# Kernel optimization log

Measured on AMD Instinct MI355X. Metric: run time of the kernel, lower is better.

Reference implementation:

```python
import jax, jax.numpy as jnp
import numpy as np
from jax import lax

# Model dims (match init_kwargs)
B, CX, XS = 32, 3, 64          # batch, x_channels, x_size
CY, K, S, Z = 32, 10, 1, 256   # y_channels, kernel_size, stride, z_size
M = (XS - K) // S + 1          # y_size = 55
FEAT = CY * M * M              # flattened y feature size
DT, TAU_X, TAU_Y = 0.1, 1.0, 0.2
BETA_Y, BETA_Z = 3.0, 7.0
STEPS = 30                     # max_num_steps
DN = ('NCHW', 'OIHW', 'NCHW')


def setup_inputs() -> dict:
    key = jax.random.key(0)
    k1, k2, k3 = jax.random.split(key, 3)
    x = jax.random.normal(k1, (B, CX, XS, XS), dtype=jnp.float32)
    # conv/convT share this kernel (torch ties convT.weight = conv.weight)
    Kw = jax.random.normal(k2, (CY, CX, K, K), dtype=jnp.float32) / np.sqrt(CX * K * K)
    # xavier_normal_ for W [Z, FEAT]
    W = jax.random.normal(k3, (Z, FEAT), dtype=jnp.float32) * np.sqrt(2.0 / (Z + FEAT))
    return {"x": x, "Kw": Kw, "W": W}


def _step(x, y, Kw, W):
    # fc: z = W @ softmax_channels(beta_y * y).flatten  -> [B, Z]
    fy = jax.nn.softmax(BETA_Y * y, axis=1)                       # softmax over channel dim
    z = jnp.einsum('zf,bf->bz', W, fy.reshape(fy.shape[0], -1))
    # nonlin_z: softmax over z-slots (dim=-2 of [B,N,1] == N axis)
    fz = jax.nn.softmax(BETA_Z * z, axis=-1)
    top = jnp.einsum('zf,bz->bf', W, fz).reshape(-1, CY, M, M)    # fcT
    conv_x = lax.conv_general_dilated(x, Kw, (S, S), 'VALID', dimension_numbers=DN)
    y_inst = conv_x + top
    y = y + DT / TAU_Y * (-y + y_inst)
    # x_instant = convT(softmax_channels(y))  (no beta here, matching the torch code)
    x_inst = lax.conv_transpose(jax.nn.softmax(y, axis=1), Kw, (S, S), 'VALID',
                                dimension_numbers=DN, transpose_kernel=True)
    x = x + DT / TAU_X * (-x + x_inst)
    return x, y


def reference(x, Kw, W):
    y0 = jnp.zeros((x.shape[0], CY, M, M), dtype=x.dtype)

    def body(carry, _):
        xc, yc = carry
        return _step(xc, yc, Kw, W), None

    (xf, _), _ = lax.scan(body, (x, y0), None, length=STEPS)
    return xf
```

## Files before the change

kernel.cpp:

```cpp
#include <hip/hip_runtime.h>

#define K_B    32
#define K_CXC  3
#define K_XS   64
#define K_CY   32
#define K_M    55
#define K_Z    256
#define K_P    (K_M*K_M)
#define K_FEAT (K_CY*K_P)
#define K_XN   (K_CXC*K_XS*K_XS)
#define K_NSPLIT 55

typedef __attribute__((ext_vector_type(8))) short short8;
typedef __attribute__((ext_vector_type(4))) float f32x4;

__device__ __forceinline__ short f2bf(float f) {
    unsigned u = __builtin_bit_cast(unsigned, f);
    unsigned r = (u + 0x7FFFu + ((u >> 16) & 1u)) >> 16;
    return (short)r;
}

__global__ __launch_bounds__(256) void w_to_bf16(const float* __restrict__ W,
                                                 short* __restrict__ Wb) {
    size_t i = ((size_t)blockIdx.x*256 + threadIdx.x) * 8;
    float4 a = *(const float4*)(W + i);
    float4 b = *(const float4*)(W + i + 4);
    short8 o;
    o[0]=f2bf(a.x); o[1]=f2bf(a.y); o[2]=f2bf(a.z); o[3]=f2bf(a.w);
    o[4]=f2bf(b.x); o[5]=f2bf(b.y); o[6]=f2bf(b.z); o[7]=f2bf(b.w);
    *(short8*)(Wb + i) = o;
}

__global__ __launch_bounds__(256) void w_to_g2(const float* __restrict__ W,
                                               short* __restrict__ Wg2) {
    int f = blockIdx.x*256 + threadIdx.x;
    if (f >= K_FEAT) return;
    int zb = blockIdx.y;
    short8 o;
    #pragma unroll
    for (int j = 0; j < 8; ++j) o[j] = f2bf(W[(size_t)(zb*8 + j)*K_FEAT + f]);
    *(short8*)(Wg2 + ((size_t)zb*K_FEAT + f)*8) = o;
}

__global__ __launch_bounds__(256) void prep_frags(const float* __restrict__ Kw,
                                                  short* __restrict__ KfragT,
                                                  short* __restrict__ Kfrag2) {
    int e = blockIdx.x*256 + threadIdx.x;
    if (e < 6400) {
        int uv = e >> 6, l = e & 63;
        int u = uv / 10, v = uv - u*10;
        int lr = l & 15, lg = l >> 4;
        short8 o;
        #pragma unroll
        for (int j = 0; j < 8; ++j) {
            int cy = lg*8 + j;
            o[j] = (lr < 3) ? f2bf(Kw[cy*300 + lr*100 + (9-u)*10 + (9-v)]) : (short)0;
        }
        *(short8*)(KfragT + (size_t)e*8) = o;
    } else if (e < 6400 + 1920) {
        int e2 = e - 6400;
        int kn = e2 >> 6, l = e2 & 63;
        int ks = kn >> 1, nt = kn & 1;
        int lr = l & 15, lg = l >> 4;
        short8 o;
        #pragma unroll
        for (int j = 0; j < 8; ++j) {
            int k = ks*32 + lg*8 + j;
            int cx = k / 160, rem = k - cx*160;
            int u = rem >> 4, v = rem & 15;
            o[j] = (v < 10) ? f2bf(Kw[(lr + nt*16)*300 + cx*100 + u*10 + v]) : (short)0;
        }
        *(short8*)(Kfrag2 + (size_t)e2*8) = o;
    }
}

__global__ __launch_bounds__(256) void fyb_fill(short* __restrict__ fyb) {
    size_t i = ((size_t)blockIdx.x*256 + threadIdx.x) * 8;
    if (i >= (size_t)K_B*K_FEAT) return;
    short8 o = {0x3D00,0x3D00,0x3D00,0x3D00,0x3D00,0x3D00,0x3D00,0x3D00};
    *(short8*)(fyb + i) = o;
}

__global__ __launch_bounds__(256) void fused_A(const float* __restrict__ x,
                                               float* __restrict__ cxb,
                                               const short* __restrict__ Wb,
                                               const short* __restrict__ fyb,
                                               float* __restrict__ zpart,
                                               const short* __restrict__ Kfrag2) {
    __shared__ __align__(16) short lds[29760];
    int bid = blockIdx.x;
    int t = threadIdx.x;
    if (bid < 512) {
        short* xcopy = lds;
        short* kf = lds + 14400;
        int b = bid >> 4, tile = bid & 15;
        int i0 = (tile >> 2) * 16, j0 = (tile & 3) * 16;
        const float* xb = x + (size_t)b*K_XN;
        for (int e = t; e < 1800; e += 256) {
            int s = e / 225, rem = e - s*225;
            int cx = rem / 75, r2 = rem - cx*75;
            int row = r2 / 3, i16 = r2 - row*3;
            int gr = i0 + row;
            int gc0 = j0 + i16*8 + s;
            const float* xp = xb + cx*4096 + gr*64;
            short8 o;
            #pragma unroll
            for (int j = 0; j < 8; ++j) {
                int gc = gc0 + j;
                float v = (gr < 64 && gc < 64) ? xp[gc] : 0.f;
                o[j] = f2bf(v);
            }
            *(short8*)(xcopy + (size_t)e*8) = o;
        }
        for (int e = t; e < 1920; e += 256)
            *(short8*)(kf + (size_t)e*8) = *(const short8*)(Kfrag2 + (size_t)e*8);
        __syncthreads();
        int wid = t >> 6, l = t & 63, lr = l & 15, lg = l >> 4;
        f32x4 acc[4][2];
        #pragma unroll
        for (int r = 0; r < 4; ++r) { acc[r][0] = (f32x4){0,0,0,0}; acc[r][1] = (f32x4){0,0,0,0}; }
        #pragma unroll 3
        for (int ks = 0; ks < 15; ++ks) {
            short8 a0 = *(const short8*)(kf + ((size_t)(ks*2+0)*64 + l)*8);
            short8 a1 = *(const short8*)(kf + ((size_t)(ks*2+1)*64 + l)*8);
            int koff = ks*32 + lg*8;
            int cx = koff / 160, rem = koff - cx*160;
            int u = rem >> 4, v0 = rem & 15;
            int w = lr + v0;
            int abase = (w & 7)*225 + cx*75 + (w >> 3);
            #pragma unroll
            for (int r = 0; r < 4; ++r) {
                int xrow = wid*4 + r + u;
                short8 bf = *(const short8*)(xcopy + (size_t)(abase + xrow*3)*8);
                acc[r][0] = __builtin_amdgcn_mfma_f32_16x16x32_bf16(a0, bf, acc[r][0], 0, 0, 0);
                acc[r][1] = __builtin_amdgcn_mfma_f32_16x16x32_bf16(a1, bf, acc[r][1], 0, 0, 0);
            }
        }
        int jcol = j0 + lr;
        bool jv = jcol < 55;
        #pragma unroll
        for (int r = 0; r < 4; ++r) {
            int ir = i0 + wid*4 + r;
            if (ir >= 55) continue;
            #pragma unroll
            for (int half = 0; half < 2; ++half) {
                #pragma unroll
                for (int rr = 0; rr < 4; ++rr) {
                    int cy = half*16 + lg*4 + rr;
                    if (jv) cxb[(size_t)b*K_FEAT + cy*K_P + ir*55 + jcol] = acc[r][half][rr];
                }
            }
        }
    } else {
        int g = bid - 512;
        int bx = g & 3, by = g >> 2;
        int wid = t >> 6, l = t & 63;
        int lr = l & 15, lg = l >> 4;
        int zi0 = bx*64 + wid*16;
        int k0  = by*1760;
        const short* Ap  = Wb  + (size_t)(zi0 + lr)*K_FEAT + k0 + lg*8;
        const short* Bp0 = fyb + (size_t)(lr)*K_FEAT      + k0 + lg*8;
        const short* Bp1 = fyb + (size_t)(16 + lr)*K_FEAT + k0 + lg*8;
        f32x4 acc0 = {0.f,0.f,0.f,0.f}, acc1 = {0.f,0.f,0.f,0.f};
        #pragma unroll 5
        for (int k = 0; k < 55; ++k) {
            short8 a  = *(const short8*)(Ap  + k*32);
            short8 b0 = *(const short8*)(Bp0 + k*32);
            short8 b1 = *(const short8*)(Bp1 + k*32);
            acc0 = __builtin_amdgcn_mfma_f32_16x16x32_bf16(a, b0, acc0, 0, 0, 0);
            acc1 = __builtin_amdgcn_mfma_f32_16x16x32_bf16(a, b1, acc1, 0, 0, 0);
        }
        float* zp = zpart + (size_t)by*8192;
        #pragma unroll
        for (int r = 0; r < 4; ++r) {
            zp[(lr)*K_Z    + zi0 + lg*4 + r] = acc0[r];
            zp[(16+lr)*K_Z + zi0 + lg*4 + r] = acc1[r];
        }
    }
}

__global__ __launch_bounds__(256) void fzk(const float* __restrict__ zpart,
                                           short* __restrict__ fzb) {
    __shared__ float sr[256];
    int b = blockIdx.x, t = threadIdx.x;
    float zv = 0.f;
    #pragma unroll 5
    for (int p = 0; p < K_NSPLIT; ++p) zv += zpart[(size_t)p*8192 + b*K_Z + t];
    float v = 7.0f * zv;
    sr[t] = v; __syncthreads();
    for (int off = 128; off > 0; off >>= 1) {
        if (t < off) sr[t] = fmaxf(sr[t], sr[t+off]);
        __syncthreads();
    }
    float m = sr[0];
    __syncthreads();
    float e = __expf(v - m);
    sr[t] = e; __syncthreads();
    for (int off = 128; off > 0; off >>= 1) {
        if (t < off) sr[t] += sr[t+off];
        __syncthreads();
    }
    float s = sr[0];
    fzb[b*K_Z + t] = f2bf(e / s);
}

__global__ __launch_bounds__(256) void gemm2_mfma(const short* __restrict__ Wg2,
                                                  const short* __restrict__ fzb,
                                                  const float* __restrict__ cxb,
                                                  float* __restrict__ y) {
    int t = threadIdx.x;
    int wid = t >> 6, l = t & 63;
    int lr = l & 15, lg = l >> 4;
    int f0 = blockIdx.x*128 + wid*32;
    if (f0 >= K_FEAT) return;
    const short* A0 = fzb + (size_t)(lr)*K_Z      + lg*8;
    const short* A1 = fzb + (size_t)(16 + lr)*K_Z + lg*8;
    short8 af0[8], af1[8];
    #pragma unroll
    for (int k = 0; k < 8; ++k) {
        af0[k] = *(const short8*)(A0 + k*32);
        af1[k] = *(const short8*)(A1 + k*32);
    }
    f32x4 acc[2][2] = {{{0.f,0.f,0.f,0.f},{0.f,0.f,0.f,0.f}},
                       {{0.f,0.f,0.f,0.f},{0.f,0.f,0.f,0.f}}};
    #pragma unroll
    for (int nt = 0; nt < 2; ++nt) {
        int f1 = f0 + nt*16;
        #pragma unroll
        for (int k = 0; k < 8; ++k) {
            const short* bp = Wg2 + ((size_t)(k*4 + lg)*K_FEAT + f1 + lr)*8;
            short8 b = *(const short8*)bp;
            acc[0][nt] = __builtin_amdgcn_mfma_f32_16x16x32_bf16(af0[k], b, acc[0][nt], 0, 0, 0);
            acc[1][nt] = __builtin_amdgcn_mfma_f32_16x16x32_bf16(af1[k], b, acc[1][nt], 0, 0, 0);
        }
    }
    #pragma unroll
    for (int mt = 0; mt < 2; ++mt) {
        #pragma unroll
        for (int nt = 0; nt < 2; ++nt) {
            #pragma unroll
            for (int r = 0; r < 4; ++r) {
                int bb = mt*16 + lg*4 + r;
                size_t idx = (size_t)bb*K_FEAT + f0 + nt*16 + lr;
                y[idx] = 0.5f*(y[idx] + cxb[idx] + acc[mt][nt][r]);
            }
        }
    }
}

__global__ __launch_bounds__(256) void softmax_dual(const float* __restrict__ y,
                                                    short* __restrict__ syb,
                                                    short* __restrict__ fyb) {
    int tid = blockIdx.x*256 + threadIdx.x;
    if (tid >= K_B*K_P) return;
    int b = tid / K_P, p = tid - b*K_P;
    const float* ip = y + (size_t)b*K_FEAT + p;
    float v[32];
    #pragma unroll
    for (int c = 0; c < 32; ++c) v[c] = ip[c*K_P];
    float m = v[0];
    #pragma unroll
    for (int c = 1; c < 32; ++c) m = fmaxf(m, v[c]);
    float e1[32];
    float s1 = 0.f, s3 = 0.f;
    #pragma unroll
    for (int c = 0; c < 32; ++c) {
        float d = v[c] - m;
        float a1 = __expf(d);
        float a3 = __expf(3.0f*d);
        e1[c] = a1; v[c] = a3;
        s1 += a1; s3 += a3;
    }
    float i1 = 1.0f/s1, i3 = 1.0f/s3;
    short* fp = fyb + (size_t)b*K_FEAT + p;
    #pragma unroll
    for (int c = 0; c < 32; ++c) fp[c*K_P] = f2bf(v[c]*i3);
    short8 o[4];
    #pragma unroll
    for (int g = 0; g < 4; ++g)
        #pragma unroll
        for (int j = 0; j < 8; ++j) o[g][j] = f2bf(e1[g*8+j]*i1);
    short* sp = syb + (size_t)tid*32;
    *(short8*)(sp)      = o[0];
    *(short8*)(sp + 8)  = o[1];
    *(short8*)(sp + 16) = o[2];
    *(short8*)(sp + 24) = o[3];
}

__global__ __launch_bounds__(256) void convT_mfma(const short* __restrict__ syb,
                                                  const short* __restrict__ KfragT,
                                                  float* __restrict__ x) {
    __shared__ __align__(16) short syt[25*41*32];
    int t = threadIdx.x;
    int tile = blockIdx.x;
    int b = blockIdx.y;
    int p0 = (tile >> 1) * 16, q0 = (tile & 1) * 32;
    for (int e = t; e < 1025; e += 256) {
        int row = e / 41, col = e - row*41;
        int gr = p0 - 9 + row, gc = q0 - 9 + col;
        short8 z = {0,0,0,0,0,0,0,0};
        short8 v0 = z, v1 = z, v2 = z, v3 = z;
        if (gr >= 0 && gr < 55 && gc >= 0 && gc < 55) {
            const short* sp = syb + ((size_t)b*K_P + gr*55 + gc) * 32;
            v0 = *(const short8*)(sp);
            v1 = *(const short8*)(sp + 8);
            v2 = *(const short8*)(sp + 16);
            v3 = *(const short8*)(sp + 24);
        }
        short* dp = syt + (size_t)e * 32;
        *(short8*)(dp)      = v0;
        *(short8*)(dp + 8)  = v1;
        *(short8*)(dp + 16) = v2;
        *(short8*)(dp + 24) = v3;
    }
    __syncthreads();
    int wid = t >> 6, l = t & 63, lr = l & 15, lg = l >> 4;
    f32x4 acc[4][2];
    #pragma unroll
    for (int r = 0; r < 4; ++r) { acc[r][0] = (f32x4){0,0,0,0}; acc[r][1] = (f32x4){0,0,0,0}; }
    const short* kfp = KfragT + (size_t)l * 8;
    for (int u = 0; u < 10; ++u) {
        #pragma unroll 5
        for (int v = 0; v < 10; ++v) {
            short8 a = *(const short8*)(kfp + (size_t)(u*10 + v)*512);
            #pragma unroll
            for (int r = 0; r < 4; ++r) {
                int rowlds = wid*4 + r + u;
                const short* bp = syt + ((size_t)(rowlds*41 + v + lr)*32 + lg*8);
                short8 b0 = *(const short8*)bp;
                short8 b1 = *(const short8*)(bp + 16*32);
                acc[r][0] = __builtin_amdgcn_mfma_f32_16x16x32_bf16(a, b0, acc[r][0], 0, 0, 0);
                acc[r][1] = __builtin_amdgcn_mfma_f32_16x16x32_bf16(a, b1, acc[r][1], 0, 0, 0);
            }
        }
    }
    if (lg == 0) {
        #pragma unroll
        for (int r = 0; r < 4; ++r) {
            int p = p0 + wid*4 + r;
            #pragma unroll
            for (int ct = 0; ct < 2; ++ct) {
                int q = q0 + ct*16 + lr;
                #pragma unroll
                for (int c = 0; c < 3; ++c) {
                    float* xp = x + (size_t)b*K_XN + c*4096 + p*64 + q;
                    *xp = 0.9f*(*xp) + 0.1f*acc[r][ct][c];
                }
            }
        }
    }
}

extern "C" void kernel_launch(void* const* d_in, const int* in_sizes, int n_in,
                              void* d_out, int out_size, void* d_ws, size_t ws_size,
                              hipStream_t stream) {
    const float* xin = (const float*)d_in[0];
    const float* Kw  = (const float*)d_in[1];
    const float* W   = (const float*)d_in[2];
    float* x = (float*)d_out;

    float* ws     = (float*)d_ws;
    float* y      = ws;
    float* cxb    = y     + 3097600;
    float* zpart  = cxb   + 3097600;
    short* fyb    = (short*)(zpart + 450560);
    short* fzb    = fyb   + 3097600;
    short* Wb     = fzb   + 8192;
    short* Wg2    = Wb    + 24780800;
    short* syb    = Wg2   + 24780800;
    short* KfragT = syb   + 3097600;
    short* Kfrag2 = KfragT+ 51200;

    hipMemcpyAsync(x, xin, (size_t)K_B*K_XN*sizeof(float), hipMemcpyDeviceToDevice, stream);
    hipMemsetAsync(y, 0, (size_t)3097600*sizeof(float), stream);
    prep_frags<<<33, 256, 0, stream>>>(Kw, KfragT, Kfrag2);
    w_to_bf16<<<12100, 256, 0, stream>>>(W, Wb);
    w_to_g2<<<dim3(379,32), 256, 0, stream>>>(W, Wg2);
    fyb_fill<<<1513, 256, 0, stream>>>(fyb);

    for (int s = 0; s < 30; ++s) {
        fused_A<<<732, 256, 0, stream>>>(x, cxb, Wb, fyb, zpart, Kfrag2);
        fzk<<<32, 256, 0, stream>>>(zpart, fzb);
        gemm2_mfma<<<757, 256, 0, stream>>>(Wg2, fzb, cxb, y);
        softmax_dual<<<379, 256, 0, stream>>>(y, syb, fyb);
        convT_mfma<<<dim3(8,32), 256, 0, stream>>>(syb, KfragT, x);
    }
}
```

Baseline: 3.206 ms.

## Switch feature layout to channel-innermost and fuse channel softmax into gemm2 epilogue

Permutes the feature axis to pixel-major, channel-innermost order (W copies, cxb, y, fyb, syb all use index p*32+cy). This lets the gemm2 epilogue compute the channel softmax with 16-lane shuffles and drop the separate softmax_dual kernel and its strided reload of y. Conv output stores become vectorized float4 writes, and fused_A reads the Kfrag2 weights straight from global memory instead of staging them in LDS. The catch is that convT must now read syb in the new layout, and the W permutation kernels do strided gathers during setup.

Result: faster. 2.829 ms (-11.8%).

```diff
diff --git a/kernel.cpp b/kernel.cpp
--- a/kernel.cpp
+++ b/kernel.cpp
@@ -20,26 +20,29 @@
     return (short)r;
 }
 
-__global__ __launch_bounds__(256) void w_to_bf16(const float* __restrict__ W,
-                                                 short* __restrict__ Wb) {
-    size_t i = ((size_t)blockIdx.x*256 + threadIdx.x) * 8;
-    float4 a = *(const float4*)(W + i);
-    float4 b = *(const float4*)(W + i + 4);
+__global__ __launch_bounds__(256) void w_perm1(const float* __restrict__ W,
+                                               short* __restrict__ Wbp) {
+    int o = blockIdx.x*256 + threadIdx.x;
+    int zi = o / 12100, c = o - zi*12100;
+    int p = c >> 2, cyg = c & 3;
+    const float* wp = W + (size_t)zi*K_FEAT + p;
+    short8 v;
+    #pragma unroll
+    for (int j = 0; j < 8; ++j) v[j] = f2bf(wp[(size_t)(cyg*8 + j)*K_P]);
+    *(short8*)(Wbp + (size_t)o*8) = v;
+}
+
+__global__ __launch_bounds__(256) void w_perm2(const float* __restrict__ W,
+                                               short* __restrict__ Wg2p) {
+    int F = blockIdx.x*256 + threadIdx.x;
+    if (F >= K_FEAT) return;
+    int zb = blockIdx.y;
+    int cy = F & 31, p = F >> 5;
     short8 o;
-    o[0]=f2bf(a.x); o[1]=f2bf(a.y); o[2]=f2bf(a.z); o[3]=f2bf(a.w);
-    o[4]=f2bf(b.x); o[5]=f2bf(b.y); o[6]=f2bf(b.z); o[7]=f2bf(b.w);
-    *(short8*)(Wb + i) = o;
-}
-
-__global__ __launch_bounds__(256) void w_to_g2(const float* __restrict__ W,
-                                               short* __restrict__ Wg2) {
-    int f = blockIdx.x*256 + threadIdx.x;
-    if (f >= K_FEAT) return;
-    int zb = blockIdx.y;
-    short8 o;
-    #pragma unroll
-    for (int j = 0; j < 8; ++j) o[j] = f2bf(W[(size_t)(zb*8 + j)*K_FEAT + f]);
-    *(short8*)(Wg2 + ((size_t)zb*K_FEAT + f)*8) = o;
+    #pragma unroll
+    for (int j = 0; j < 8; ++j)
+        o[j] = f2bf(W[(size_t)(zb*8 + j)*K_FEAT + cy*K_P + p]);
+    *(short8*)(Wg2p + ((size_t)zb*K_FEAT + F)*8) = o;
 }
 
 __global__ __launch_bounds__(256) void prep_frags(const float* __restrict__ Kw,
@@ -83,16 +86,14 @@
 
 __global__ __launch_bounds__(256) void fused_A(const float* __restrict__ x,
                                                float* __restrict__ cxb,
-                                               const short* __restrict__ Wb,
+                                               const short* __restrict__ Wbp,
                                                const short* __restrict__ fyb,
                                                float* __restrict__ zpart,
                                                const short* __restrict__ Kfrag2) {
-    __shared__ __align__(16) short lds[29760];
+    __shared__ __align__(16) short xcopy[14400];
     int bid = blockIdx.x;
     int t = threadIdx.x;
     if (bid < 512) {
-        short* xcopy = lds;
-        short* kf = lds + 14400;
         int b = bid >> 4, tile = bid & 15;
         int i0 = (tile >> 2) * 16, j0 = (tile & 3) * 16;
         const float* xb = x + (size_t)b*K_XN;
@@ -112,8 +113,6 @@
             }
             *(short8*)(xcopy + (size_t)e*8) = o;
         }
-        for (int e = t; e < 1920; e += 256)
-            *(short8*)(kf + (size_t)e*8) = *(const short8*)(Kfrag2 + (size_t)e*8);
         __syncthreads();
         int wid = t >> 6, l = t & 63, lr = l & 15, lg = l >> 4;
         f32x4 acc[4][2];
@@ -121,8 +120,8 @@
         for (int r = 0; r < 4; ++r) { acc[r][0] = (f32x4){0,0,0,0}; acc[r][1] = (f32x4){0,0,0,0}; }
         #pragma unroll 3
         for (int ks = 0; ks < 15; ++ks) {
-            short8 a0 = *(const short8*)(kf + ((size_t)(ks*2+0)*64 + l)*8);
-            short8 a1 = *(const short8*)(kf + ((size_t)(ks*2+1)*64 + l)*8);
+            short8 a0 = *(const short8*)(Kfrag2 + ((size_t)(ks*2+0)*64 + l)*8);
+            short8 a1 = *(const short8*)(Kfrag2 + ((size_t)(ks*2+1)*64 + l)*8);
             int koff = ks*32 + lg*8;
             int cx = koff / 160, rem = koff - cx*160;
             int u = rem >> 4, v0 = rem & 15;
@@ -141,15 +140,10 @@
         #pragma unroll
         for (int r = 0; r < 4; ++r) {
             int ir = i0 + wid*4 + r;
-            if (ir >= 55) continue;
-            #pragma unroll
-            for (int half = 0; half < 2; ++half) {
-                #pragma unroll
-                for (int rr = 0; rr < 4; ++rr) {
-                    int cy = half*16 + lg*4 + rr;
-                    if (jv) cxb[(size_t)b*K_FEAT + cy*K_P + ir*55 + jcol] = acc[r][half][rr];
-                }
-            }
+            if (ir >= 55 || !jv) continue;
+            size_t base = (size_t)b*K_FEAT + (size_t)(ir*55 + jcol)*32 + lg*4;
+            *(f32x4*)&cxb[base]      = acc[r][0];
+            *(f32x4*)&cxb[base + 16] = acc[r][1];
         }
     } else {
         int g = bid - 512;
@@ -158,7 +152,7 @@
         int lr = l & 15, lg = l >> 4;
         int zi0 = bx*64 + wid*16;
         int k0  = by*1760;
-        const short* Ap  = Wb  + (size_t)(zi0 + lr)*K_FEAT + k0 + lg*8;
+        const short* Ap  = Wbp + (size_t)(zi0 + lr)*K_FEAT + k0 + lg*8;
         const short* Bp0 = fyb + (size_t)(lr)*K_FEAT      + k0 + lg*8;
         const short* Bp1 = fyb + (size_t)(16 + lr)*K_FEAT + k0 + lg*8;
         f32x4 acc0 = {0.f,0.f,0.f,0.f}, acc1 = {0.f,0.f,0.f,0.f};
@@ -204,15 +198,18 @@
     fzb[b*K_Z + t] = f2bf(e / s);
 }
 
-__global__ __launch_bounds__(256) void gemm2_mfma(const short* __restrict__ Wg2,
-                                                  const short* __restrict__ fzb,
-                                                  const float* __restrict__ cxb,
-                                                  float* __restrict__ y) {
+__global__ __launch_bounds__(256) void gemm2_sm(const short* __restrict__ Wg2p,
+                                                const short* __restrict__ fzb,
+                                                const float* __restrict__ cxb,
+                                                float* __restrict__ y,
+                                                short* __restrict__ syb,
+                                                short* __restrict__ fyb) {
     int t = threadIdx.x;
     int wid = t >> 6, l = t & 63;
     int lr = l & 15, lg = l >> 4;
     int f0 = blockIdx.x*128 + wid*32;
-    if (f0 >= K_FEAT) return;
+    int p = f0 >> 5;
+    if (p >= K_P) return;
     const short* A0 = fzb + (size_t)(lr)*K_Z      + lg*8;
     const short* A1 = fzb + (size_t)(16 + lr)*K_Z + lg*8;
     short8 af0[8], af1[8];
@@ -225,10 +222,9 @@
                        {{0.f,0.f,0.f,0.f},{0.f,0.f,0.f,0.f}}};
     #pragma unroll
     for (int nt = 0; nt < 2; ++nt) {
-        int f1 = f0 + nt*16;
         #pragma unroll
         for (int k = 0; k < 8; ++k) {
-            const short* bp = Wg2 + ((size_t)(k*4 + lg)*K_FEAT + f1 + lr)*8;
+            const short* bp = Wg2p + ((size_t)(k*4 + lg)*K_FEAT + f0 + nt*16 + lr)*8;
             short8 b = *(const short8*)bp;
             acc[0][nt] = __builtin_amdgcn_mfma_f32_16x16x32_bf16(af0[k], b, acc[0][nt], 0, 0, 0);
             acc[1][nt] = __builtin_amdgcn_mfma_f32_16x16x32_bf16(af1[k], b, acc[1][nt], 0, 0, 0);
@@ -237,54 +233,27 @@
     #pragma unroll
     for (int mt = 0; mt < 2; ++mt) {
         #pragma unroll
-        for (int nt = 0; nt < 2; ++nt) {
-            #pragma unroll
-            for (int r = 0; r < 4; ++r) {
-                int bb = mt*16 + lg*4 + r;
-                size_t idx = (size_t)bb*K_FEAT + f0 + nt*16 + lr;
-                y[idx] = 0.5f*(y[idx] + cxb[idx] + acc[mt][nt][r]);
-            }
-        }
-    }
-}
-
-__global__ __launch_bounds__(256) void softmax_dual(const float* __restrict__ y,
-                                                    short* __restrict__ syb,
-                                                    short* __restrict__ fyb) {
-    int tid = blockIdx.x*256 + threadIdx.x;
-    if (tid >= K_B*K_P) return;
-    int b = tid / K_P, p = tid - b*K_P;
-    const float* ip = y + (size_t)b*K_FEAT + p;
-    float v[32];
-    #pragma unroll
-    for (int c = 0; c < 32; ++c) v[c] = ip[c*K_P];
-    float m = v[0];
-    #pragma unroll
-    for (int c = 1; c < 32; ++c) m = fmaxf(m, v[c]);
-    float e1[32];
-    float s1 = 0.f, s3 = 0.f;
-    #pragma unroll
-    for (int c = 0; c < 32; ++c) {
-        float d = v[c] - m;
-        float a1 = __expf(d);
-        float a3 = __expf(3.0f*d);
-        e1[c] = a1; v[c] = a3;
-        s1 += a1; s3 += a3;
-    }
-    float i1 = 1.0f/s1, i3 = 1.0f/s3;
-    short* fp = fyb + (size_t)b*K_FEAT + p;
-    #pragma unroll
-    for (int c = 0; c < 32; ++c) fp[c*K_P] = f2bf(v[c]*i3);
-    short8 o[4];
-    #pragma unroll
-    for (int g = 0; g < 4; ++g)
-        #pragma unroll
-        for (int j = 0; j < 8; ++j) o[g][j] = f2bf(e1[g*8+j]*i1);
-    short* sp = syb + (size_t)tid*32;
-    *(short8*)(sp)      = o[0];
-    *(short8*)(sp + 8)  = o[1];
-    *(short8*)(sp + 16) = o[2];
-    *(short8*)(sp + 24) = o[3];
+        for (int r = 0; r < 4; ++r) {
+            int bb = mt*16 + lg*4 + r;
+            size_t i0a = (size_t)bb*K_FEAT + f0 + lr;
+            size_t i1a = i0a + 16;
+            float v0 = 0.5f*(y[i0a] + cxb[i0a] + acc[mt][0][r]);
+            float v1 = 0.5f*(y[i1a] + cxb[i1a] + acc[mt][1][r]);
+            float mx = fmaxf(v0, v1);
+            #pragma unroll
+            for (int m = 1; m <= 8; m <<= 1) mx = fmaxf(mx, __shfl_xor(mx, m));
+            float d0 = v0 - mx, d1 = v1 - mx;
+            float e10 = __expf(d0),      e11 = __expf(d1);
+            float e30 = __expf(3.0f*d0), e31 = __expf(3.0f*d1);
+            float s1 = e10 + e11, s3 = e30 + e31;
+            #pragma unroll
+            for (int m = 1; m <= 8; m <<= 1) { s1 += __shfl_xor(s1, m); s3 += __shfl_xor(s3, m); }
+            float i1 = 1.0f/s1, i3 = 1.0f/s3;
+            y[i0a] = v0; y[i1a] = v1;
+            syb[i0a] = f2bf(e10*i1); syb[i1a] = f2bf(e11*i1);
+            fyb[i0a] = f2bf(e30*i3); fyb[i1a] = f2bf(e31*i3);
+        }
+    }
 }
 
 __global__ __launch_bounds__(256) void convT_mfma(const short* __restrict__ syb,
@@ -365,24 +334,23 @@
     float* zpart  = cxb   + 3097600;
     short* fyb    = (short*)(zpart + 450560);
     short* fzb    = fyb   + 3097600;
-    short* Wb     = fzb   + 8192;
-    short* Wg2    = Wb    + 24780800;
-    short* syb    = Wg2   + 24780800;
+    short* Wbp    = fzb   + 8192;
+    short* Wg2p   = Wbp   + 24780800;
+    short* syb    = Wg2p  + 24780800;
     short* KfragT = syb   + 3097600;
     short* Kfrag2 = KfragT+ 51200;
 
     hipMemcpyAsync(x, xin, (size_t)K_B*K_XN*sizeof(float), hipMemcpyDeviceToDevice, stream);
     hipMemsetAsync(y, 0, (size_t)3097600*sizeof(float), stream);
     prep_frags<<<33, 256, 0, stream>>>(Kw, KfragT, Kfrag2);
-    w_to_bf16<<<12100, 256, 0, stream>>>(W, Wb);
-    w_to_g2<<<dim3(379,32), 256, 0, stream>>>(W, Wg2);
+    w_perm1<<<12100, 256, 0, stream>>>(W, Wbp);
+    w_perm2<<<dim3(379,32), 256, 0, stream>>>(W, Wg2p);
     fyb_fill<<<1513, 256, 0, stream>>>(fyb);
 
     for (int s = 0; s < 30; ++s) {
-        fused_A<<<732, 256, 0, stream>>>(x, cxb, Wb, fyb, zpart, Kfrag2);
+        fused_A<<<732, 256, 0, stream>>>(x, cxb, Wbp, fyb, zpart, Kfrag2);
         fzk<<<32, 256, 0, stream>>>(zpart, fzb);
-        gemm2_mfma<<<757, 256, 0, stream>>>(Wg2, fzb, cxb, y);
-        softmax_dual<<<379, 256, 0, stream>>>(y, syb, fyb);
+        gemm2_sm<<<757, 256, 0, stream>>>(Wg2p, fzb, cxb, y, syb, fyb);
         convT_mfma<<<dim3(8,32), 256, 0, stream>>>(syb, KfragT, x);
     }
 }
```
